# Performance work log

Measured on AMD Instinct MI355X. Metric: run time of the kernel, lower is better.

## Reference

```python
import jax, jax.numpy as jnp
import numpy as np

B, K, V, D, T = 8, 4, 32000, 1024, 16
EOS, PAD = 2, 0
EOS_SCORE = 1000.0
BIG = 1e9  # suppresses beams 1..K-1 at step 0 (original starts from a single beam)


def setup_inputs() -> dict:
    key = jax.random.key(0)
    k1, k2, k3, k4 = jax.random.split(key, 4)
    s = 1.0 / np.sqrt(D)
    return {
        "words": jnp.ones((B, K), dtype=jnp.int32),  # BOS=1 on every beam
        "h0": jnp.zeros((B, K, D), dtype=jnp.float32),
        "c0": jnp.zeros((B, K, D), dtype=jnp.float32),
        "E": jax.random.normal(k1, (V, D), dtype=jnp.float32) * s,
        "Wx": jax.random.normal(k2, (D, 4 * D), dtype=jnp.float32) * s,
        "Wh": jax.random.normal(k3, (D, 4 * D), dtype=jnp.float32) * s,
        "b": jnp.zeros((4 * D,), dtype=jnp.float32),
        "Wout": jax.random.normal(k4, (D, V), dtype=jnp.float32) * s,
        "bout": jnp.zeros((V,), dtype=jnp.float32),
    }


def reference(words, h0, c0, E, Wx, Wh, b, Wout, bout):
    bidx = jnp.arange(B)[:, None]
    kidx = jnp.arange(K)[None, :]
    scores0 = jnp.concatenate(
        [jnp.zeros((B, 1), jnp.float32), jnp.full((B, K - 1), BIG, jnp.float32)], axis=1)
    buf0 = jnp.zeros((B, K, T), dtype=jnp.int32)
    stopped0 = jnp.zeros((B,), dtype=bool)

    def step(carry, j):
        w, scores, h, c, stopped, buf = carry
        # proc_word: embed -> LSTM cell -> vocab logits (vectorized over B*K beams)
        x = E[w]                                              # [B,K,D]
        gates = jnp.einsum('bkd,df->bkf', x, Wx) + jnp.einsum('bkd,df->bkf', h, Wh) + b
        i_, f_, g_, o_ = jnp.split(gates, 4, axis=-1)
        c_new = jax.nn.sigmoid(f_) * c + jax.nn.sigmoid(i_) * jnp.tanh(g_)
        h_new = jax.nn.sigmoid(o_) * jnp.tanh(c_new)
        logits = jnp.einsum('bkd,dv->bkv', h_new, Wout) + bout  # [B,K,V]
        p = -jax.nn.log_softmax(logits, axis=-1)                # negative log-probs
        neg_ps, idxs = jax.lax.top_k(-p, K)                     # K smallest per beam
        cand = (-neg_ps) + scores[:, :, None]                   # [B,K,K]
        flat = cand.reshape(B, K * K)
        wflat = idxs.reshape(B, K * K)
        neg_sel, sel = jax.lax.top_k(-flat, K)                  # K smallest over all cands
        sel_scores = -neg_sel                                   # [B,K]
        prev = sel // K                                         # originating beam
        new_w = jnp.take_along_axis(wflat, sel, axis=1)
        eos = new_w == EOS
        first_eos = eos[:, 0] & (~stopped)                      # best cand is EOS -> stop
        pen = eos & (~first_eos[:, None]) & (~stopped[:, None]) # non-best EOS penalized
        sel_scores = jnp.where(pen, EOS_SCORE, sel_scores)
        tok = jnp.where(first_eos[:, None], EOS, new_w)
        tok = jnp.where(stopped[:, None], PAD, tok)
        prevb = jnp.where(stopped[:, None], kidx, prev)         # stopped rows keep order
        buf = buf[bidx, prevb]                                  # reorder beam histories
        buf = buf.at[:, :, j].set(tok.astype(jnp.int32))
        h_new = h_new[bidx, prev]                               # gather per-beam states
        c_new = c_new[bidx, prev]
        scores = jnp.where(stopped[:, None], scores, sel_scores)
        w = jnp.where(stopped[:, None], w, new_w.astype(w.dtype))
        stopped = stopped | first_eos
        return (w, scores, h_new, c_new, stopped, buf), None

    carry0 = (words, scores0, h0, c0, stopped0, buf0)
    (_, scores, _, _, _, buf), _ = jax.lax.scan(step, carry0, jnp.arange(T))
    return buf, scores
```

## Files before the change

kernel.cpp:

```cpp
#include <hip/hip_runtime.h>
#include <math.h>
#include <float.h>

namespace {

constexpr int Bb = 8, Kk = 4, BKn = 32, Dd = 1024, Ff = 4096, Vv = 32000, Tt = 16;
constexpr int GDS = 8;
constexpr int LTW = 64;
constexpr int LNB = Vv / LTW;
constexpr int LQC = 16;
constexpr int LQN = 16;
constexpr int NVCH = LNB;
constexpr int EOSt = 2, PADt = 0;
constexpr float BIGf = 1e9f, EOSSf = 1000.0f;

constexpr size_t OFF_HTN = 0;
constexpr size_t OFF_CB0 = OFF_HTN + (size_t)Dd * BKn;
constexpr size_t OFF_CB1 = OFF_CB0 + (size_t)BKn * Dd;
constexpr size_t OFF_GP  = OFF_CB1 + (size_t)BKn * Dd;
constexpr size_t OFF_CS  = OFF_GP  + (size_t)GDS * BKn * Ff;
constexpr size_t OFF_SC  = OFF_CS  + (size_t)NVCH * BKn * 12;
constexpr size_t OFF_INT = OFF_SC  + BKn;
constexpr int IW = 0, ISTOP = 32, IPREV = 40, IBUFA = 72, IBUFB = IBUFA + Bb * Kk * Tt;

__device__ __forceinline__ void cp16(const float* g, float* l) {
  __builtin_amdgcn_global_load_lds(
      (const __attribute__((address_space(1))) void*)g,
      (__attribute__((address_space(3))) void*)l, 16, 0, 0);
}

__device__ inline void ins4(float v, int id, float tv[4], int ti[4]) {
#pragma unroll
  for (int r = 0; r < 4; r++) {
    bool better = (v > tv[r]) || (v == tv[r] && id < ti[r]);
    if (better) { float fv = tv[r]; int fi = ti[r]; tv[r] = v; ti[r] = id; v = fv; id = fi; }
  }
}

template <int STARTOFF>
__device__ inline void merge_top4(float tv[4], int ti[4], float ov[4], int oi[4]) {
#pragma unroll
  for (int r = 0; r < 4; r++) {
    float hv = tv[0]; int hi = ti[0];
    float m = hv;
    for (int off = STARTOFF; off; off >>= 1) m = fmaxf(m, __shfl_xor(m, off));
    int c = (hv == m) ? hi : 0x7fffffff;
    for (int off = STARTOFF; off; off >>= 1) c = min(c, __shfl_xor(c, off));
    if (hv == m && hi == c) {
      tv[0] = tv[1]; ti[0] = ti[1];
      tv[1] = tv[2]; ti[1] = ti[2];
      tv[2] = tv[3]; ti[2] = ti[3];
      tv[3] = -FLT_MAX; ti[3] = 0x7fffffff;
    }
    ov[r] = m; oi[r] = c;
  }
}

__global__ __launch_bounds__(256) void initK(const int* __restrict__ words,
    const float* __restrict__ h0, const float* __restrict__ c0,
    float* __restrict__ ws) {
  int* wsi = (int*)(ws + OFF_INT);
  if (blockIdx.x < 128) {
    int g = blockIdx.x * 256 + threadIdx.x;
    int d = g >> 5, bk = g & 31;
    ws[OFF_HTN + g] = h0[(size_t)bk * Dd + d];
    ws[OFF_CB0 + g] = c0[g];
  } else {
    int t = threadIdx.x;
    if (t < BKn) {
      ws[OFF_SC + t] = ((t & 3) == 0) ? 0.f : BIGf;
      wsi[IW + t] = words[t];
      wsi[IPREV + t] = t & 3;
    }
    if (t < Bb) wsi[ISTOP + t] = 0;
    for (int i = t; i < 2 * Bb * Kk * Tt; i += 256) wsi[IBUFA + i] = 0;
  }
}

__global__ __launch_bounds__(256) void gatesAK(const float* __restrict__ Wx,
    const float* __restrict__ Wh, const float* __restrict__ E,
    const float* __restrict__ hTn, const int* __restrict__ wsi,
    float* __restrict__ Gp) {
  __shared__ float wxb[4][3][4][64];
  __shared__ float whb[4][3][4][64];
  __shared__ float xs[128][BKn];
  __shared__ float hs[128][BKn];
  __shared__ float sd[BKn][64];
  int tid = threadIdx.x;
  int q = tid >> 6;
  int lane = tid & 63;
  int cg = lane & 15;
  int bg = lane >> 4;
  int f0 = blockIdx.x * 64;
  int dblk0 = blockIdx.y * 128;

  {
    int bk = tid & 31, dq = tid >> 5;
    int w = wsi[IW + bk];
    int src = (bk & ~3) | wsi[IPREV + bk];
    const float* Erow = E + (size_t)w * Dd + dblk0;
#pragma unroll
    for (int k = 0; k < 16; k++) {
      int d = dq * 16 + k;
      xs[d][bk] = Erow[d];
      hs[d][bk] = hTn[(size_t)(dblk0 + d) * BKn + src];
    }
  }
  __syncthreads();

  float acc[4][8];
#pragma unroll
  for (int c = 0; c < 4; c++)
#pragma unroll
    for (int i = 0; i < 8; i++) acc[c][i] = 0.f;

#define STAGE(CH, B)                                                          \
  {                                                                           \
    int gd_ = dblk0 + q * 32 + (CH) * 4 + (lane >> 4);                        \
    cp16(Wx + (size_t)gd_ * Ff + f0 + (lane & 15) * 4, &wxb[q][B][0][0]);     \
    cp16(Wh + (size_t)gd_ * Ff + f0 + (lane & 15) * 4, &whb[q][B][0][0]);     \
  }

  STAGE(0, 0)
  STAGE(1, 1)
  for (int k = 0; k < 8; k++) {
    int b = k % 3;
    if (k + 2 < 8) {
      STAGE(k + 2, (k + 2) % 3)
      asm volatile("s_waitcnt vmcnt(4)" ::: "memory");
    } else if (k + 1 < 8) {
      asm volatile("s_waitcnt vmcnt(2)" ::: "memory");
    } else {
      asm volatile("s_waitcnt vmcnt(0)" ::: "memory");
    }
    __builtin_amdgcn_sched_barrier(0);
    int ldb = q * 32 + k * 4;
#pragma unroll
    for (int d = 0; d < 4; d++) {
      float4 wx4 = *(const float4*)&wxb[q][b][d][cg * 4];
      float4 wh4 = *(const float4*)&whb[q][b][d][cg * 4];
      float4 xlo = *(const float4*)&xs[ldb + d][bg * 8];
      float4 xhi = *(const float4*)&xs[ldb + d][bg * 8 + 4];
      float4 hlo = *(const float4*)&hs[ldb + d][bg * 8];
      float4 hhi = *(const float4*)&hs[ldb + d][bg * 8 + 4];
      float wxc[4] = {wx4.x, wx4.y, wx4.z, wx4.w};
      float whc[4] = {wh4.x, wh4.y, wh4.z, wh4.w};
      float xv[8] = {xlo.x, xlo.y, xlo.z, xlo.w, xhi.x, xhi.y, xhi.z, xhi.w};
      float hv[8] = {hlo.x, hlo.y, hlo.z, hlo.w, hhi.x, hhi.y, hhi.z, hhi.w};
#pragma unroll
      for (int c = 0; c < 4; c++)
#pragma unroll
        for (int i = 0; i < 8; i++)
          acc[c][i] = fmaf(xv[i], wxc[c], fmaf(hv[i], whc[c], acc[c][i]));
    }
  }
#undef STAGE

  if (q == 0) {
#pragma unroll
    for (int c = 0; c < 4; c++)
#pragma unroll
      for (int i = 0; i < 8; i++)
        sd[bg * 8 + i][cg * 4 + c] = acc[c][i];
  }
  __syncthreads();
#pragma unroll
  for (int qq = 1; qq < 4; qq++) {
    if (q == qq) {
#pragma unroll
      for (int c = 0; c < 4; c++)
#pragma unroll
        for (int i = 0; i < 8; i++)
          sd[bg * 8 + i][cg * 4 + c] += acc[c][i];
    }
    __syncthreads();
  }

  {
    int row = tid >> 3, c8 = tid & 7;
    float* dst = Gp + ((size_t)blockIdx.y * BKn + row) * Ff + f0 + c8 * 8;
    *(float4*)dst       = *(const float4*)&sd[row][c8 * 8];
    *(float4*)(dst + 4) = *(const float4*)&sd[row][c8 * 8 + 4];
  }
}

__global__ __launch_bounds__(256) void lstmK(const float* __restrict__ bvec,
    const float* __restrict__ Gp, const float* __restrict__ cPrev,
    const int* __restrict__ wsi, float* __restrict__ cNew,
    float* __restrict__ hTn) {
  __shared__ float part[4][128];
  int bk = blockIdx.x;
  int dcl = threadIdx.x & 127;
  int half = threadIdx.x >> 7;
  int dc = blockIdx.y * 128 + dcl;
  float s[4] = {0.f, 0.f, 0.f, 0.f};
#pragma unroll
  for (int dsl = 0; dsl < 4; dsl++) {
    int ds = half * 4 + dsl;
    const float* row = Gp + ((size_t)ds * BKn + bk) * Ff;
#pragma unroll
    for (int g = 0; g < 4; g++) s[g] += row[(size_t)g * Dd + dc];
  }
  if (half == 1) {
#pragma unroll
    for (int g = 0; g < 4; g++) part[g][dcl] = s[g];
  }
  __syncthreads();
  if (half == 0) {
    float gi = s[0] + part[0][dcl] + bvec[dc];
    float gf = s[1] + part[1][dcl] + bvec[Dd + dc];
    float gg = s[2] + part[2][dcl] + bvec[2 * Dd + dc];
    float go = s[3] + part[3][dcl] + bvec[3 * Dd + dc];
    int src = (bk & ~3) | wsi[IPREV + bk];
    float c = cPrev[(size_t)src * Dd + dc];
    float si = 1.f / (1.f + expf(-gi));
    float sf = 1.f / (1.f + expf(-gf));
    float so = 1.f / (1.f + expf(-go));
    float tg = tanhf(gg);
    float cn = sf * c + si * tg;
    float hn = so * tanhf(cn);
    cNew[(size_t)bk * Dd + dc] = cn;
    hTn[(size_t)dc * BKn + bk] = hn;
  }
}

__global__ __launch_bounds__(256) void logitsAK(const float* __restrict__ Wo,
    const float* __restrict__ bo, const float* __restrict__ hTn,
    float* __restrict__ cs) {
  __shared__ float wb[4][3][LQC][LTW];
  __shared__ float hb[4][3][LQC][BKn];
  __shared__ float sd[BKn][LTW];
  int tid = threadIdx.x;
  int q = tid >> 6;
  int lane = tid & 63;
  int cg = lane & 15;
  int bg = lane >> 4;
  size_t v0 = (size_t)blockIdx.x * LTW;
  int dq0 = q * 256;
  float acc[4][8];
#pragma unroll
  for (int c = 0; c < 4; c++)
#pragma unroll
    for (int i = 0; i < 8; i++) acc[c][i] = 0.f;

  float4 b4 = *(const float4*)(bo + v0 + cg * 4);

#define STAGE(CH, B)                                                          \
  {                                                                           \
    int d0_ = dq0 + (CH) * LQC;                                               \
    _Pragma("unroll") for (int i_ = 0; i_ < 4; i_++)                          \
      cp16(Wo + (size_t)(d0_ + i_ * 4 + (lane >> 4)) * Vv + v0 +              \
               (lane & 15) * 4,                                               \
           &wb[q][B][i_ * 4][0]);                                             \
    _Pragma("unroll") for (int j_ = 0; j_ < 2; j_++)                          \
      cp16(hTn + (size_t)(d0_ + j_ * 8 + (lane >> 3)) * BKn + (lane & 7) * 4, \
           &hb[q][B][j_ * 8][0]);                                             \
  }

  STAGE(0, 0)
  STAGE(1, 1)
  for (int k = 0; k < LQN; k++) {
    int b = k % 3;
    if (k + 2 < LQN) {
      STAGE(k + 2, (k + 2) % 3)
      asm volatile("s_waitcnt vmcnt(12)" ::: "memory");
    } else if (k + 1 < LQN) {
      asm volatile("s_waitcnt vmcnt(6)" ::: "memory");
    } else {
      asm volatile("s_waitcnt vmcnt(0)" ::: "memory");
    }
    __builtin_amdgcn_sched_barrier(0);
#pragma unroll 4
    for (int d = 0; d < LQC; d++) {
      float4 w4  = *(const float4*)&wb[q][b][d][cg * 4];
      float4 hlo = *(const float4*)&hb[q][b][d][bg * 8];
      float4 hhi = *(const float4*)&hb[q][b][d][bg * 8 + 4];
      float wv[4] = {w4.x, w4.y, w4.z, w4.w};
      float hv[8] = {hlo.x, hlo.y, hlo.z, hlo.w, hhi.x, hhi.y, hhi.z, hhi.w};
#pragma unroll
      for (int c = 0; c < 4; c++)
#pragma unroll
        for (int i = 0; i < 8; i++)
          acc[c][i] = fmaf(wv[c], hv[i], acc[c][i]);
    }
  }
#undef STAGE

  float bb[4] = {b4.x, b4.y, b4.z, b4.w};
  if (q == 0) {
#pragma unroll
    for (int c = 0; c < 4; c++)
#pragma unroll
      for (int i = 0; i < 8; i++)
        sd[bg * 8 + i][cg * 4 + c] = acc[c][i] + bb[c];
  }
  __syncthreads();
#pragma unroll
  for (int qq = 1; qq < 4; qq++) {
    if (q == qq) {
#pragma unroll
      for (int c = 0; c < 4; c++)
#pragma unroll
        for (int i = 0; i < 8; i++)
          sd[bg * 8 + i][cg * 4 + c] += acc[c][i];
    }
    __syncthreads();
  }

  int i0 = (int)v0 + lane;
  for (int bb_ = 0; bb_ < 8; ++bb_) {
    int bk = q * 8 + bb_;
    float v0f = sd[bk][lane];
    float m = v0f;
    for (int off = 32; off; off >>= 1) m = fmaxf(m, __shfl_xor(m, off));
    float se = expf(v0f - m);
    for (int off = 32; off; off >>= 1) se += __shfl_xor(se, off);
    float tv[4]; int ti[4];
#pragma unroll
    for (int r = 0; r < 4; r++) { tv[r] = -FLT_MAX; ti[r] = 0x7fffffff; }
    ins4(v0f, i0, tv, ti);
    float ov[4]; int oi[4];
    merge_top4<32>(tv, ti, ov, oi);
    if (lane == 0) {
      float* p = cs + ((size_t)blockIdx.x * BKn + bk) * 12;
      p[0] = m; p[1] = se;
#pragma unroll
      for (int r = 0; r < 4; r++) { p[2 + r] = ov[r]; p[6 + r] = __int_as_float(oi[r]); }
    }
  }
}

__global__ __launch_bounds__(1024) void redSelK(float* __restrict__ ws, int step) {
  __shared__ float bt_s[BKn][8];
  __shared__ int s_tok[BKn], s_prevb[BKn];
  int* wsi = (int*)(ws + OFF_INT);
  const float* cs = ws + OFF_CS;
  int tid = threadIdx.x;
  int wv = tid >> 6, lane = tid & 63;
  {
    int half = lane >> 5, l32 = lane & 31;
    int bk = wv * 2 + half;
    float tv[4]; int ti[4];
#pragma unroll
    for (int r = 0; r < 4; r++) { tv[r] = -FLT_MAX; ti[r] = 0x7fffffff; }
    float M = -FLT_MAX, ls = 0.f;
    for (int g = 0; g < 4; g++) {
      float4 pa[4], pb[4], pc[4];
      bool vv[4];
#pragma unroll
      for (int j = 0; j < 4; j++) {
        int c = l32 + 32 * (g * 4 + j);
        vv[j] = c < NVCH;
        const float* p = cs + ((size_t)c * BKn + bk) * 12;
        if (vv[j]) {
          pa[j] = *(const float4*)p;
          pb[j] = *(const float4*)(p + 4);
          pc[j] = *(const float4*)(p + 8);
        }
      }
#pragma unroll
      for (int j = 0; j < 4; j++) {
        if (vv[j]) {
          float cm = pa[j].x, csum = pa[j].y;
          if (cm > M) { ls *= expf(M - cm); M = cm; }
          ls += csum * expf(cm - M);
          ins4(pa[j].z, __float_as_int(pb[j].z), tv, ti);
          ins4(pa[j].w, __float_as_int(pb[j].w), tv, ti);
          ins4(pb[j].x, __float_as_int(pc[j].x), tv, ti);
          ins4(pb[j].y, __float_as_int(pc[j].y), tv, ti);
        }
      }
    }
    for (int off = 16; off; off >>= 1) {
      float Mo = __shfl_xor(M, off), lso = __shfl_xor(ls, off);
      float Mn = fmaxf(M, Mo);
      ls = ls * expf(M - Mn) + lso * expf(Mo - Mn);
      M = Mn;
    }
    float lse = M + logf(ls);
    float ov[4]; int oi[4];
    merge_top4<16>(tv, ti, ov, oi);
    if (l32 == 0) {
#pragma unroll
      for (int r = 0; r < 4; r++) {
        bt_s[bk][r] = lse - ov[r];
        bt_s[bk][4 + r] = __int_as_float(oi[r]);
      }
    }
  }
  __syncthreads();
  if (tid < Bb) {
    int b = tid;
    int st = wsi[ISTOP + b];
    float sc[4];
#pragma unroll
    for (int k = 0; k < 4; k++) sc[k] = ws[OFF_SC + b * 4 + k];
    float cval[16]; int ctok[16];
#pragma unroll
    for (int kb = 0; kb < 4; kb++)
#pragma unroll
      for (int r = 0; r < 4; r++) {
        cval[kb * 4 + r] = bt_s[b * 4 + kb][r] + sc[kb];
        ctok[kb * 4 + r] = __float_as_int(bt_s[b * 4 + kb][4 + r]);
      }
    float selS[4]; int selW[4], prevK[4];
    int usedMask = 0;
#pragma unroll
    for (int r = 0; r < 4; r++) {
      int best = -1; float bv = FLT_MAX;
#pragma unroll
      for (int t = 0; t < 16; t++) {
        if (!((usedMask >> t) & 1) && cval[t] < bv) { bv = cval[t]; best = t; }
      }
      usedMask |= 1 << best;
      int tok = 0;
#pragma unroll
      for (int t = 0; t < 16; t++) if (t == best) tok = ctok[t];
      selS[r] = bv; selW[r] = tok; prevK[r] = best >> 2;
    }
    bool eos[4];
#pragma unroll
    for (int r = 0; r < 4; r++) eos[r] = (selW[r] == EOSt);
    bool first = eos[0] && !st;
#pragma unroll
    for (int r = 0; r < 4; r++) if (eos[r] && !first && !st) selS[r] = EOSSf;
#pragma unroll
    for (int k = 0; k < 4; k++) {
      int tok = st ? PADt : (first ? EOSt : selW[k]);
      int pb  = st ? k : prevK[k];
      s_tok[b * 4 + k] = tok;
      s_prevb[b * 4 + k] = pb;
      if (!st) { ws[OFF_SC + b * 4 + k] = selS[k]; wsi[IW + b * 4 + k] = selW[k]; }
      wsi[IPREV + b * 4 + k] = prevK[k];
    }
    wsi[ISTOP + b] = (st || first) ? 1 : 0;
  }
  __syncthreads();
  if (tid < 512) {
    const int* br = wsi + (((step & 1) == 0) ? IBUFA : IBUFB);
    int* bw = wsi + (((step & 1) == 0) ? IBUFB : IBUFA);
    int bkk = tid >> 4, t = tid & 15;
    int pb = s_prevb[bkk];
    int src = ((bkk & ~3) | pb) * Tt + t;
    int val = br[src];
    if (t == step) val = s_tok[bkk];
    bw[tid] = val;
  }
}

__global__ __launch_bounds__(256) void outK(const float* __restrict__ ws,
                                            float* __restrict__ out) {
  const int* wsi = (const int*)(ws + OFF_INT);
  int g = blockIdx.x * 256 + threadIdx.x;
  if (g < Bb * Kk * Tt) {
    out[g] = (float)wsi[IBUFA + g];
  } else if (g < Bb * Kk * Tt + BKn) {
    out[g] = ws[OFF_SC + (g - Bb * Kk * Tt)];
  }
}

}

extern "C" void kernel_launch(void* const* d_in, const int* in_sizes, int n_in,
                              void* d_out, int out_size, void* d_ws, size_t ws_size,
                              hipStream_t stream) {
  (void)in_sizes; (void)n_in; (void)out_size; (void)ws_size;
  const int*   words = (const int*)d_in[0];
  const float* h0 = (const float*)d_in[1];
  const float* c0 = (const float*)d_in[2];
  const float* E  = (const float*)d_in[3];
  const float* Wx = (const float*)d_in[4];
  const float* Wh = (const float*)d_in[5];
  const float* bv = (const float*)d_in[6];
  const float* Wo = (const float*)d_in[7];
  const float* bo = (const float*)d_in[8];
  float* ws = (float*)d_ws;
  float* hTn = ws + OFF_HTN;
  float* cb0 = ws + OFF_CB0;
  float* cb1 = ws + OFF_CB1;
  float* Gp  = ws + OFF_GP;
  float* cs  = ws + OFF_CS;
  int*   wsi = (int*)(ws + OFF_INT);

  initK<<<129, 256, 0, stream>>>(words, h0, c0, ws);
  for (int j = 0; j < Tt; j++) {
    float* cPrev = (j & 1) ? cb1 : cb0;
    float* cNext = (j & 1) ? cb0 : cb1;
    gatesAK<<<dim3(64, GDS), 256, 0, stream>>>(Wx, Wh, E, hTn, wsi, Gp);
    lstmK<<<dim3(32, 8), 256, 0, stream>>>(bv, Gp, cPrev, wsi, cNext, hTn);
    logitsAK<<<LNB, 256, 0, stream>>>(Wo, bo, hTn, cs);
    redSelK<<<1, 1024, 0, stream>>>(ws, j);
  }
  outK<<<3, 256, 0, stream>>>(ws, (float*)d_out);
}
```

Measured before the change: 1.664 ms.

## Repack output weight matrix into contiguous per-block tiles with non-temporal loads

Adds a one-time kernel that transposes Wout into a blocked layout where each 64-column vocab tile has all 1024 rows stored contiguously. The logits kernel then streams its weights linearly instead of with strided 64-wide row segments, and uses a non-temporal cache hint on those loads. The aim is better DRAM and TLB locality for the weight stream, which dominates logits time. The cost is an extra 131 MB read/write pass per call for the repack, which every decode step must amortize.

Result: slower. 1.767 ms (+6.2%).

```diff
diff --git a/kernel.cpp b/kernel.cpp
--- a/kernel.cpp
+++ b/kernel.cpp
@@ -22,11 +22,18 @@
 constexpr size_t OFF_SC  = OFF_CS  + (size_t)NVCH * BKn * 12;
 constexpr size_t OFF_INT = OFF_SC  + BKn;
 constexpr int IW = 0, ISTOP = 32, IPREV = 40, IBUFA = 72, IBUFB = IBUFA + Bb * Kk * Tt;
+constexpr size_t OFF_PWO = OFF_INT + 2048;
 
 __device__ __forceinline__ void cp16(const float* g, float* l) {
   __builtin_amdgcn_global_load_lds(
       (const __attribute__((address_space(1))) void*)g,
       (__attribute__((address_space(3))) void*)l, 16, 0, 0);
+}
+
+__device__ __forceinline__ void cp16nt(const float* g, float* l) {
+  __builtin_amdgcn_global_load_lds(
+      (const __attribute__((address_space(1))) void*)g,
+      (__attribute__((address_space(3))) void*)l, 16, 0, 2);
 }
 
 __device__ inline void ins4(float v, int id, float tv[4], int ti[4]) {
@@ -74,6 +81,33 @@
     }
     if (t < Bb) wsi[ISTOP + t] = 0;
     for (int i = t; i < 2 * Bb * Kk * Tt; i += 256) wsi[IBUFA + i] = 0;
+  }
+}
+
+__global__ __launch_bounds__(256) void packWoK(const float* __restrict__ Wo,
+                                               float* __restrict__ pwo) {
+  __shared__ float tile[32][256];
+  int t = threadIdx.x;
+  int v0 = blockIdx.x * 256;
+  int d0 = blockIdx.y * 32;
+  int rs = t >> 6;
+  int lane = t & 63;
+#pragma unroll
+  for (int p = 0; p < 8; p++) {
+    int r = p * 4 + rs;
+    *(float4*)&tile[r][lane * 4] =
+        *(const float4*)(Wo + (size_t)(d0 + r) * Vv + v0 + lane * 4);
+  }
+  __syncthreads();
+  int tb = rs;
+  int b = (v0 >> 6) + tb;
+  float* dst = pwo + ((size_t)b * Dd + d0) * 64;
+#pragma unroll
+  for (int p = 0; p < 8; p++) {
+    int off = p * 256 + lane * 4;
+    int dd = off >> 6;
+    int cc = off & 63;
+    *(float4*)(dst + off) = *(const float4*)&tile[dd][tb * 64 + cc];
   }
 }
 
@@ -224,7 +258,7 @@
   }
 }
 
-__global__ __launch_bounds__(256) void logitsAK(const float* __restrict__ Wo,
+__global__ __launch_bounds__(256) void logitsAK(const float* __restrict__ pwo,
     const float* __restrict__ bo, const float* __restrict__ hTn,
     float* __restrict__ cs) {
   __shared__ float wb[4][3][LQC][LTW];
@@ -237,6 +271,7 @@
   int bg = lane >> 4;
   size_t v0 = (size_t)blockIdx.x * LTW;
   int dq0 = q * 256;
+  const float* wbase = pwo + (size_t)blockIdx.x * Dd * 64;
   float acc[4][8];
 #pragma unroll
   for (int c = 0; c < 4; c++)
@@ -249,9 +284,8 @@
   {                                                                           \
     int d0_ = dq0 + (CH) * LQC;                                               \
     _Pragma("unroll") for (int i_ = 0; i_ < 4; i_++)                          \
-      cp16(Wo + (size_t)(d0_ + i_ * 4 + (lane >> 4)) * Vv + v0 +              \
-               (lane & 15) * 4,                                               \
-           &wb[q][B][i_ * 4][0]);                                             \
+      cp16nt(wbase + (size_t)(d0_ + i_ * 4) * 64 + lane * 4,                  \
+             &wb[q][B][i_ * 4][0]);                                           \
     _Pragma("unroll") for (int j_ = 0; j_ < 2; j_++)                          \
       cp16(hTn + (size_t)(d0_ + j_ * 8 + (lane >> 3)) * BKn + (lane & 7) * 4, \
            &hb[q][B][j_ * 8][0]);                                             \
@@ -480,15 +514,17 @@
   float* cb1 = ws + OFF_CB1;
   float* Gp  = ws + OFF_GP;
   float* cs  = ws + OFF_CS;
+  float* pwo = ws + OFF_PWO;
   int*   wsi = (int*)(ws + OFF_INT);
 
   initK<<<129, 256, 0, stream>>>(words, h0, c0, ws);
+  packWoK<<<dim3(125, 32), 256, 0, stream>>>(Wo, pwo);
   for (int j = 0; j < Tt; j++) {
     float* cPrev = (j & 1) ? cb1 : cb0;
     float* cNext = (j & 1) ? cb0 : cb1;
     gatesAK<<<dim3(64, GDS), 256, 0, stream>>>(Wx, Wh, E, hTn, wsi, Gp);
     lstmK<<<dim3(32, 8), 256, 0, stream>>>(bv, Gp, cPrev, wsi, cNext, hTn);
-    logitsAK<<<LNB, 256, 0, stream>>>(Wo, bo, hTn, cs);
+    logitsAK<<<LNB, 256, 0, stream>>>(pwo, bo, hTn, cs);
     redSelK<<<1, 1024, 0, stream>>>(ws, j);
   }
   outK<<<3, 256, 0, stream>>>(ws, (float*)d_out);
```
